# Optimization experiments

Hardware: AMD Instinct MI355X
Metric: run time of the kernel (lower is better)

## Reference

```python
import jax, jax.numpy as jnp
import numpy as np

B, H, W, C = 64, 32, 32, 256
HZ, WZ = 16, 16
N = 64          # hidden_dim = n_proposals
K = 3           # dynamic depthwise kernel size
EPS = 1e-5


def _layernorm(x, g, b):
    mu = jnp.mean(x, axis=-1, keepdims=True)
    var = jnp.var(x, axis=-1, keepdims=True)
    return (x - mu) * jax.lax.rsqrt(var + EPS) * g + b


def setup_inputs() -> dict:
    key = jax.random.key(0)
    ks = jax.random.split(key, 8)
    s = 0.02  # weight init scale
    return {
        "x_feat": jax.random.normal(ks[0], (B, H, W, C), jnp.float32),
        "z_feat": jax.random.normal(ks[1], (B, HZ, WZ, C), jnp.float32),
        "Wz": jax.random.normal(ks[2], (C, N), jnp.float32) * s,
        "bz": jnp.zeros((N,), jnp.float32),
        "Wx": jax.random.normal(ks[3], (C, N), jnp.float32) * s,
        "bx": jnp.zeros((N,), jnp.float32),
        "Wdyn": jax.random.normal(ks[4], (C, N + K), jnp.float32) * s,
        "bdyn": jnp.zeros((N + K,), jnp.float32),
        "g_norm": jnp.ones((C,), jnp.float32),
        "b_norm": jnp.zeros((C,), jnp.float32),
        "Wp": jax.random.normal(ks[5], (C, 1), jnp.float32) * s,
        "bp": jnp.zeros((1,), jnp.float32),
        "g_ln": jnp.ones((C,), jnp.float32),
        "b_ln": jnp.zeros((C,), jnp.float32),
    }


def _dysep_conv_atten(query, value, Wdyn, bdyn, g_norm, b_norm):
    # query, value: [B, N, C]
    dy = query @ Wdyn + bdyn                      # [B, N, N+K]
    w_depth = dy[:, :, :K]                        # [B, N, K] per-channel depthwise kernels
    w_point = dy[:, :, K:]                        # [B, N, N] per-sample pointwise (1x1) weights
    # depthwise conv along C with 'same' padding (torch conv1d = cross-correlation)
    vpad = jnp.pad(value, ((0, 0), (0, 0), (1, 1)))
    depth = (w_depth[..., 0:1] * vpad[:, :, 0:C]
             + w_depth[..., 1:2] * vpad[:, :, 1:C + 1]
             + w_depth[..., 2:3] * vpad[:, :, 2:C + 2])
    depth = jax.nn.relu(depth)                    # [B, N, C]
    point = jnp.einsum('bnm,bmc->bnc', w_point, depth)
    return _layernorm(point, g_norm, b_norm)


def reference(x_feat, z_feat, Wz, bz, Wx, bx, Wdyn, bdyn,
              g_norm, b_norm, Wp, bp, g_ln, b_ln):
    # kernels from template features (detached in the original: kernels.detach())
    z_core = z_feat @ Wz + bz                                   # [B,HZ,WZ,N]
    kernels = jnp.einsum('bhwn,bhwc->bnc', z_core, z_feat)      # [B,N,C]
    kernels = jax.lax.stop_gradient(kernels)

    x_n = x_feat @ Wx + bx                                      # [B,H,W,N]
    kernels_x = jnp.einsum('bhwn,bhwc->bnc', x_n, x_feat)       # [B,N,C]
    kernels_x = _dysep_conv_atten(kernels, kernels_x, Wdyn, bdyn, g_norm, b_norm)

    x_corr = jnp.einsum('bnc,bhwn->bhwc', kernels_x, x_n)       # [B,H,W,C]
    proto = kernels_x @ Wp + bp                                 # [B,N,1]
    tem = jax.nn.sigmoid(jnp.einsum('bnd,bnc->bdc', proto, kernels_x))  # [B,1,C]
    tem = tem[:, :, None, :]                                    # [B,1,1,C]
    x_corr = x_corr * tem

    return x_feat + jax.nn.relu(_layernorm(x_corr, g_ln, b_ln))
```

## Files before the change

### kernel.cpp

```cpp
#include <hip/hip_runtime.h>
#include <math.h>

#define EPSV 1e-5f

typedef __attribute__((ext_vector_type(8))) short short8;
typedef __attribute__((ext_vector_type(4))) float f32x4;

static __device__ __forceinline__ unsigned bfpack2(float lo, float hi) {
    union { float f; unsigned u; } a, b;
    a.f = lo; b.f = hi;
    unsigned ua = a.u + 0x7fffu + ((a.u >> 16) & 1u);
    unsigned ub = b.u + 0x7fffu + ((b.u >> 16) & 1u);
    return (ua >> 16) | (ub & 0xffff0000u);
}

__global__ __launch_bounds__(256) void gram(
    const float* __restrict__ Xx, const float* __restrict__ Xz,
    float* __restrict__ Gx, float* __restrict__ Gz,
    float* __restrict__ csx, float* __restrict__ csz)
{
    __shared__ __align__(16) unsigned short AT[128 * 72];
    __shared__ __align__(16) unsigned short BT[128 * 72];
    __shared__ float csr[8 * 128];
    int id = blockIdx.x;
    const float* X; float* G; float* cs; int P;
    if (id < 192) { X = Xx; G = Gx; cs = csx; P = 1024; }
    else { id -= 192; X = Xz; G = Gz; cs = csz; P = 256; }
    const int b = id & 63;
    const int tile = id >> 6;
    const int ci = (tile == 1) ? 1 : 0;
    const int cj = (tile == 0) ? 0 : 1;
    const bool diag = (tile < 2);
    const int nk = P >> 6;
    const int t = threadIdx.x;
    const int cq = (t & 31) * 4;
    const int ph = t >> 5;
    const float* Xb = X + (long)b * P * 256;

    const int w = t >> 6;
    const int wr = w >> 1, wc = w & 1;
    const int quad = (t >> 4) & 3, lane16 = t & 15;

    f32x4 acc[4][4] = {};
    float csA[4] = {0.f, 0.f, 0.f, 0.f};

    for (int kc = 0; kc < nk; ++kc) {
        const int p0 = kc * 64 + ph * 8;
        float4 va[8], vb[8];
#pragma unroll
        for (int k = 0; k < 8; ++k)
            va[k] = *(const float4*)(Xb + (long)(p0 + k) * 256 + ci * 128 + cq);
        if (!diag) {
#pragma unroll
            for (int k = 0; k < 8; ++k)
                vb[k] = *(const float4*)(Xb + (long)(p0 + k) * 256 + cj * 128 + cq);
        }
        __syncthreads();
#pragma unroll
        for (int j = 0; j < 4; ++j) {
            uint4 pk;
            pk.x = bfpack2(((const float*)&va[0])[j], ((const float*)&va[1])[j]);
            pk.y = bfpack2(((const float*)&va[2])[j], ((const float*)&va[3])[j]);
            pk.z = bfpack2(((const float*)&va[4])[j], ((const float*)&va[5])[j]);
            pk.w = bfpack2(((const float*)&va[6])[j], ((const float*)&va[7])[j]);
            *(uint4*)&AT[(cq + j) * 72 + ph * 8] = pk;
            if (diag) {
                csA[j] += ((const float*)&va[0])[j] + ((const float*)&va[1])[j]
                        + ((const float*)&va[2])[j] + ((const float*)&va[3])[j]
                        + ((const float*)&va[4])[j] + ((const float*)&va[5])[j]
                        + ((const float*)&va[6])[j] + ((const float*)&va[7])[j];
            }
        }
        if (!diag) {
#pragma unroll
            for (int j = 0; j < 4; ++j) {
                uint4 pk;
                pk.x = bfpack2(((const float*)&vb[0])[j], ((const float*)&vb[1])[j]);
                pk.y = bfpack2(((const float*)&vb[2])[j], ((const float*)&vb[3])[j]);
                pk.z = bfpack2(((const float*)&vb[4])[j], ((const float*)&vb[5])[j]);
                pk.w = bfpack2(((const float*)&vb[6])[j], ((const float*)&vb[7])[j]);
                *(uint4*)&BT[(cq + j) * 72 + ph * 8] = pk;
            }
        }
        __syncthreads();
        const unsigned short* Br = diag ? AT : BT;
#pragma unroll
        for (int ks = 0; ks < 2; ++ks) {
            const int ko = ks * 32 + quad * 8;
            short8 bfrag[4];
#pragma unroll
            for (int ni = 0; ni < 4; ++ni)
                bfrag[ni] = *(const short8*)&Br[(wc * 64 + ni * 16 + lane16) * 72 + ko];
#pragma unroll
            for (int mi = 0; mi < 4; ++mi) {
                short8 afrag = *(const short8*)&AT[(wr * 64 + mi * 16 + lane16) * 72 + ko];
#pragma unroll
                for (int ni = 0; ni < 4; ++ni)
                    acc[mi][ni] = __builtin_amdgcn_mfma_f32_16x16x32_bf16(afrag, bfrag[ni], acc[mi][ni], 0, 0, 0);
            }
        }
    }
#pragma unroll
    for (int mi = 0; mi < 4; ++mi) {
        const int rbase = ci * 128 + wr * 64 + mi * 16 + quad * 4;
#pragma unroll
        for (int ni = 0; ni < 4; ++ni) {
            const int col = cj * 128 + wc * 64 + ni * 16 + lane16;
#pragma unroll
            for (int r = 0; r < 4; ++r) {
                G[((long)(b * 256 + rbase + r)) * 256 + col] = acc[mi][ni][r];
                if (!diag)
                    G[((long)(b * 256 + col)) * 256 + rbase + r] = acc[mi][ni][r];
            }
        }
    }
    if (diag) {
#pragma unroll
        for (int j = 0; j < 4; ++j) csr[ph * 128 + cq + j] = csA[j];
        __syncthreads();
        if (t < 128) {
            float s = 0.f;
#pragma unroll
            for (int k = 0; k < 8; ++k) s += csr[k * 128 + t];
            cs[b * 256 + ci * 128 + t] = s;
        }
    }
}

__global__ __launch_bounds__(256) void proj(
    const float* __restrict__ Gx, const float* __restrict__ csx,
    const float* __restrict__ Wx, const float* __restrict__ bx,
    float* __restrict__ kxr,
    const float* __restrict__ Gz, const float* __restrict__ csz,
    const float* __restrict__ Wz, const float* __restrict__ bz,
    float* __restrict__ kern)
{
    __shared__ __align__(16) unsigned short ATW[64 * 264];
    __shared__ __align__(16) unsigned short BTC[64 * 72];
    const int t = threadIdx.x;
    const int id = blockIdx.x;
    const int b = id & 63, s = id >> 6;
    const float *G, *cs, *W, *bias; float* O;
    if (s < 4) { G = Gx; cs = csx; W = Wx; bias = bx; O = kxr; }
    else       { G = Gz; cs = csz; W = Wz; bias = bz; O = kern; }
    const int ct = s & 3;
    const int n = t & 63, ph = t >> 6;
#pragma unroll
    for (int cc = 0; cc < 4; ++cc) {
        float v[16];
#pragma unroll
        for (int k = 0; k < 16; ++k) v[k] = W[(ph * 64 + cc * 16 + k) * 64 + n];
        uint4 p0, p1;
        p0.x = bfpack2(v[0], v[1]);   p0.y = bfpack2(v[2], v[3]);
        p0.z = bfpack2(v[4], v[5]);   p0.w = bfpack2(v[6], v[7]);
        p1.x = bfpack2(v[8], v[9]);   p1.y = bfpack2(v[10], v[11]);
        p1.z = bfpack2(v[12], v[13]); p1.w = bfpack2(v[14], v[15]);
        *(uint4*)&ATW[n * 264 + ph * 64 + cc * 16]     = p0;
        *(uint4*)&ATW[n * 264 + ph * 64 + cc * 16 + 8] = p1;
    }
    const int row = t >> 2, cq = t & 3;
    const int w = t >> 6, quad = (t >> 4) & 3, lane16 = t & 15;
    const float* Grow = G + ((long)(b * 256 + ct * 64 + row)) * 256 + cq * 16;
    f32x4 acc[4] = {{0.f,0.f,0.f,0.f},{0.f,0.f,0.f,0.f},{0.f,0.f,0.f,0.f},{0.f,0.f,0.f,0.f}};
    for (int kc = 0; kc < 4; ++kc) {
        float4 g0 = *(const float4*)(Grow + kc * 64 + 0);
        float4 g1 = *(const float4*)(Grow + kc * 64 + 4);
        float4 g2 = *(const float4*)(Grow + kc * 64 + 8);
        float4 g3 = *(const float4*)(Grow + kc * 64 + 12);
        uint4 pk0, pk1;
        pk0.x = bfpack2(g0.x, g0.y); pk0.y = bfpack2(g0.z, g0.w);
        pk0.z = bfpack2(g1.x, g1.y); pk0.w = bfpack2(g1.z, g1.w);
        pk1.x = bfpack2(g2.x, g2.y); pk1.y = bfpack2(g2.z, g2.w);
        pk1.z = bfpack2(g3.x, g3.y); pk1.w = bfpack2(g3.z, g3.w);
        __syncthreads();
        *(uint4*)&BTC[row * 72 + cq * 16]     = pk0;
        *(uint4*)&BTC[row * 72 + cq * 16 + 8] = pk1;
        __syncthreads();
#pragma unroll
        for (int ks = 0; ks < 2; ++ks) {
            const int ko = ks * 32 + quad * 8;
            short8 bfrag = *(const short8*)&BTC[(w * 16 + lane16) * 72 + ko];
#pragma unroll
            for (int mi = 0; mi < 4; ++mi) {
                short8 afrag = *(const short8*)&ATW[(mi * 16 + lane16) * 264 + kc * 64 + ko];
                acc[mi] = __builtin_amdgcn_mfma_f32_16x16x32_bf16(afrag, bfrag, acc[mi], 0, 0, 0);
            }
        }
    }
    const int col = ct * 64 + w * 16 + lane16;
    const float csv = cs[b * 256 + col];
#pragma unroll
    for (int mi = 0; mi < 4; ++mi) {
        const int nrow = mi * 16 + quad * 4;
#pragma unroll
        for (int r = 0; r < 4; ++r)
            O[((long)(b * 64 + nrow + r)) * 256 + col] = acc[mi][r] + bias[nrow + r] * csv;
    }
}

__global__ __launch_bounds__(256) void dy_all(
    const float* __restrict__ kern, const float* __restrict__ Wdyn,
    const float* __restrict__ bdyn, float* __restrict__ dyb)
{
    __shared__ float Ac[16 * 64];
    __shared__ float Wc[16 * 64];
    __shared__ float Wd3[48];
    const int b = blockIdx.x, t = threadIdx.x;
    const int tr = t >> 4, tc = t & 15;
    float acc[4][4];
#pragma unroll
    for (int j = 0; j < 4; ++j) {
        float bj = bdyn[3 + tc * 4 + j];
        acc[0][j] = bj; acc[1][j] = bj; acc[2][j] = bj; acc[3][j] = bj;
    }
    const int lr = t >> 2, lc = (t & 3) * 4;
    const int wl = t >> 4, wj = (t & 15) * 4;
    const int nwd = t / 3, jwd = t - nwd * 3;
    float wdacc = 0.f;
    float4 av = *(const float4*)(kern + ((long)(b * 64 + lr)) * 256 + lc);
    float w0 = Wdyn[wl * 67 + 3 + wj + 0];
    float w1 = Wdyn[wl * 67 + 3 + wj + 1];
    float w2 = Wdyn[wl * 67 + 3 + wj + 2];
    float w3 = Wdyn[wl * 67 + 3 + wj + 3];
    float wdr = (t < 48) ? Wdyn[(t / 3) * 67 + (t % 3)] : 0.f;

    for (int c0 = 0; c0 < 256; c0 += 16) {
        Ac[(lc+0)*64 + lr] = av.x; Ac[(lc+1)*64 + lr] = av.y;
        Ac[(lc+2)*64 + lr] = av.z; Ac[(lc+3)*64 + lr] = av.w;
        Wc[wl*64 + wj+0] = w0; Wc[wl*64 + wj+1] = w1;
        Wc[wl*64 + wj+2] = w2; Wc[wl*64 + wj+3] = w3;
        if (t < 48) Wd3[t] = wdr;
        __syncthreads();
        if (c0 + 16 < 256) {
            av = *(const float4*)(kern + ((long)(b * 64 + lr)) * 256 + c0 + 16 + lc);
            w0 = Wdyn[(c0 + 16 + wl) * 67 + 3 + wj + 0];
            w1 = Wdyn[(c0 + 16 + wl) * 67 + 3 + wj + 1];
            w2 = Wdyn[(c0 + 16 + wl) * 67 + 3 + wj + 2];
            w3 = Wdyn[(c0 + 16 + wl) * 67 + 3 + wj + 3];
            if (t < 48) wdr = Wdyn[(c0 + 16 + t / 3) * 67 + (t % 3)];
        }
#pragma unroll
        for (int cl = 0; cl < 16; ++cl) {
            float4 a = *(float4*)&Ac[cl * 64 + tr * 4];
            float4 w = *(float4*)&Wc[cl * 64 + tc * 4];
            acc[0][0]+=a.x*w.x; acc[0][1]+=a.x*w.y; acc[0][2]+=a.x*w.z; acc[0][3]+=a.x*w.w;
            acc[1][0]+=a.y*w.x; acc[1][1]+=a.y*w.y; acc[1][2]+=a.y*w.z; acc[1][3]+=a.y*w.w;
            acc[2][0]+=a.z*w.x; acc[2][1]+=a.z*w.y; acc[2][2]+=a.z*w.z; acc[2][3]+=a.z*w.w;
            acc[3][0]+=a.w*w.x; acc[3][1]+=a.w*w.y; acc[3][2]+=a.w*w.z; acc[3][3]+=a.w*w.w;
        }
        if (t < 192) {
#pragma unroll
            for (int cl = 0; cl < 16; ++cl)
                wdacc += Ac[cl * 64 + nwd] * Wd3[cl * 3 + jwd];
        }
        __syncthreads();
    }
#pragma unroll
    for (int i = 0; i < 4; ++i) {
        float4 o = make_float4(acc[i][0], acc[i][1], acc[i][2], acc[i][3]);
        *(float4*)(dyb + ((long)(b * 64 + tr * 4 + i)) * 68 + tc * 4) = o;
    }
    if (t < 192) dyb[((long)(b * 64 + nwd)) * 68 + 64 + jwd] = wdacc + bdyn[jwd];
}

__global__ __launch_bounds__(256) void depthpoint(
    const float* __restrict__ dyb, const float* __restrict__ v,
    const float* __restrict__ g, const float* __restrict__ Wp,
    float* __restrict__ point, float* __restrict__ partials)
{
    __shared__ float smem[13312];
    float* wpT = smem;
    float* wd3 = smem + 4352;
    float* vt  = smem + 4608;
    float* dep = smem + 8960;
    float* rs  = vt;

    const int t = threadIdx.x;
    const int b = blockIdx.y, ct = blockIdx.x, c0 = ct * 64;
    const int tr = t >> 4, tc = t & 15;

#pragma unroll
    for (int i = 0; i < 4; ++i) {
        int idx = t + i * 256; int n = idx >> 4, m0 = (idx & 15) * 4;
        float4 w4 = *(const float4*)(dyb + ((long)(b * 64 + n)) * 68 + m0);
        wpT[(m0+0)*68 + n] = w4.x; wpT[(m0+1)*68 + n] = w4.y;
        wpT[(m0+2)*68 + n] = w4.z; wpT[(m0+3)*68 + n] = w4.w;
    }
    if (t < 64) {
        long o = ((long)(b * 64 + t)) * 68 + 64;
        wd3[t*4+0] = dyb[o+0]; wd3[t*4+1] = dyb[o+1]; wd3[t*4+2] = dyb[o+2];
    }
    {
        int m = t >> 2, lc0 = (t & 3) * 17;
#pragma unroll
        for (int k = 0; k < 17; ++k) {
            int lc = lc0 + k;
            if (lc < 66) {
                int c = c0 - 1 + lc;
                vt[m * 68 + lc] = (c >= 0 && c < 256) ? v[((long)(b * 64 + m)) * 256 + c] : 0.f;
            }
        }
    }
    __syncthreads();
#pragma unroll
    for (int im = 0; im < 4; ++im) {
        int m = tr * 4 + im;
        float w0 = wd3[m*4+0], w1 = wd3[m*4+1], w2 = wd3[m*4+2];
#pragma unroll
        for (int jc = 0; jc < 4; ++jc) {
            int cl = tc * 4 + jc;
            float d = w0 * vt[m*68 + cl] + w1 * vt[m*68 + cl + 1] + w2 * vt[m*68 + cl + 2];
            dep[m*68 + cl] = fmaxf(d, 0.f);
        }
    }
    __syncthreads();
    float acc[4][4] = {};
#pragma unroll 16
    for (int m = 0; m < 64; ++m) {
        float4 a4 = *(float4*)&wpT[m * 68 + tr * 4];
        float4 d4 = *(float4*)&dep[m * 68 + tc * 4];
        acc[0][0]+=a4.x*d4.x; acc[0][1]+=a4.x*d4.y; acc[0][2]+=a4.x*d4.z; acc[0][3]+=a4.x*d4.w;
        acc[1][0]+=a4.y*d4.x; acc[1][1]+=a4.y*d4.y; acc[1][2]+=a4.y*d4.z; acc[1][3]+=a4.y*d4.w;
        acc[2][0]+=a4.z*d4.x; acc[2][1]+=a4.z*d4.y; acc[2][2]+=a4.z*d4.z; acc[2][3]+=a4.z*d4.w;
        acc[3][0]+=a4.w*d4.x; acc[3][1]+=a4.w*d4.y; acc[3][2]+=a4.w*d4.z; acc[3][3]+=a4.w*d4.w;
    }
    int cg = c0 + tc * 4;
    float4 g4  = *(const float4*)(g + cg);
    float4 wp4 = *(const float4*)(Wp + cg);
    float gw0 = g4.x*wp4.x, gw1 = g4.y*wp4.y, gw2 = g4.z*wp4.z, gw3 = g4.w*wp4.w;
#pragma unroll
    for (int i = 0; i < 4; ++i) {
        float4 o = make_float4(acc[i][0], acc[i][1], acc[i][2], acc[i][3]);
        *(float4*)(point + ((long)(b * 64 + tr * 4 + i)) * 256 + cg) = o;
        float s  = o.x + o.y + o.z + o.w;
        float s2 = o.x*o.x + o.y*o.y + o.z*o.z + o.w*o.w;
        float dg = o.x*gw0 + o.y*gw1 + o.z*gw2 + o.w*gw3;
        rs[0*1088 + (tr*4+i)*17 + tc] = s;
        rs[1*1088 + (tr*4+i)*17 + tc] = s2;
        rs[2*1088 + (tr*4+i)*17 + tc] = dg;
    }
    __syncthreads();
    if (t < 64) {
        float s = 0.f, s2 = 0.f, dg = 0.f;
#pragma unroll
        for (int j = 0; j < 16; ++j) {
            s  += rs[t*17 + j];
            s2 += rs[1088 + t*17 + j];
            dg += rs[2176 + t*17 + j];
        }
        long base = ((long)(b * 4 + ct)) * 192;
        partials[base + t]        = s;
        partials[base + 64 + t]   = s2;
        partials[base + 128 + t]  = dg;
    }
}

__global__ __launch_bounds__(256) void lntem(
    const float* __restrict__ partials, const float* __restrict__ point,
    const float* __restrict__ g, const float* __restrict__ bta,
    const float* __restrict__ Wp, const float* __restrict__ bp,
    float* __restrict__ murr, float* __restrict__ AB)
{
    __shared__ float sA[256], sB[256];
    __shared__ float wnv[64];
    __shared__ float tot[4];
    const int b = blockIdx.x, t = threadIdx.x;
    const int c = t;
    float gc = g[c], bc = bta[c], wpc = Wp[c];
    sA[t] = gc * wpc; sB[t] = bc * wpc;
    __syncthreads();
    for (int off = 128; off >= 1; off >>= 1) {
        if (t < off) { sA[t] += sA[t+off]; sB[t] += sB[t+off]; }
        __syncthreads();
    }
    if (t == 0) { tot[0] = sA[0]; tot[1] = sB[0] + bp[0]; }
    __syncthreads();
    float Sgw = tot[0], Sbw = tot[1];

    float protoe = 0.f, mu = 0.f, rr = 0.f;
    if (t < 64) {
        float S1 = 0.f, S2 = 0.f, Sdg = 0.f;
#pragma unroll
        for (int ct = 0; ct < 4; ++ct) {
            long o = ((long)(b * 4 + ct)) * 192;
            S1 += partials[o + t]; S2 += partials[o + 64 + t]; Sdg += partials[o + 128 + t];
        }
        mu = S1 * (1.f / 256.f);
        float var = S2 * (1.f / 256.f) - mu * mu;
        rr = rsqrtf(var + EPSV);
        protoe = rr * (Sdg - mu * Sgw) + Sbw;
        wnv[t] = protoe * rr;
        murr[b * 128 + 2*t]     = rr;
        murr[b * 128 + 2*t + 1] = -mu * rr;
    }
    __syncthreads();
    sA[t] = (t < 64) ? protoe * rr * mu : 0.f;
    sB[t] = (t < 64) ? protoe : 0.f;
    __syncthreads();
    for (int off = 128; off >= 1; off >>= 1) {
        if (t < off) { sA[t] += sA[t+off]; sB[t] += sB[t+off]; }
        __syncthreads();
    }
    if (t == 0) { tot[2] = sA[0]; tot[3] = sB[0]; }
    __syncthreads();
    float Bv = tot[2], Sv = tot[3];

    const float* pcol = point + (long)b * 64 * 256 + c;
    float a0 = 0.f, a1 = 0.f, a2 = 0.f, a3 = 0.f;
#pragma unroll
    for (int n = 0; n < 64; n += 4) {
        a0 += wnv[n+0] * pcol[(n+0) * 256];
        a1 += wnv[n+1] * pcol[(n+1) * 256];
        a2 += wnv[n+2] * pcol[(n+2) * 256];
        a3 += wnv[n+3] * pcol[(n+3) * 256];
    }
    float accA = a0 + a1 + a2 + a3;
    float x = gc * (accA - Bv) + bc * Sv;
    float temv = 1.f / (1.f + expf(-x));
    AB[b * 512 + c]       = gc * temv;
    AB[b * 512 + 256 + c] = bc * temv;
}

__global__ __launch_bounds__(256) void buildM(
    const float* __restrict__ point, const float* __restrict__ murr,
    const float* __restrict__ AB, const float* __restrict__ Wx,
    const float* __restrict__ bx,
    unsigned short* __restrict__ MT, float* __restrict__ svec)
{
    __shared__ float ks_s[64 * 68];
    __shared__ float wt_s[64 * 68];
    const int t = threadIdx.x;
    const int id = blockIdx.x;
    const int b = id & 63, mt = id >> 6;
    {
        const int n = t >> 2, q = t & 3;
        const float rn = murr[b * 128 + 2 * n], qn = murr[b * 128 + 2 * n + 1];
        const float* prow = point + ((long)(b * 64 + n)) * 256 + mt * 64 + q * 16;
        const float* Arow = AB + b * 512 + mt * 64 + q * 16;
#pragma unroll
        for (int j = 0; j < 4; ++j) {
            float4 p4 = *(const float4*)(prow + j * 4);
            float4 A4 = *(const float4*)(Arow + j * 4);
            float4 B4 = *(const float4*)(Arow + 256 + j * 4);
            float4 kv;
            kv.x = (p4.x * rn + qn) * A4.x + B4.x;
            kv.y = (p4.y * rn + qn) * A4.y + B4.y;
            kv.z = (p4.z * rn + qn) * A4.z + B4.z;
            kv.w = (p4.w * rn + qn) * A4.w + B4.w;
            *(float4*)&ks_s[n * 68 + q * 16 + j * 4] = kv;
        }
    }
    __syncthreads();
    if (t < 64) {
        float sv = 0.f;
#pragma unroll
        for (int n2 = 0; n2 < 64; ++n2) sv += bx[n2] * ks_s[n2 * 68 + t];
        svec[b * 256 + mt * 64 + t] = sv;
    }
    const int tr = t >> 4, tc = t & 15;
    const int nw = t & 63, ph = t >> 6;
    for (int cc = 0; cc < 4; ++cc) {
        float wv[16];
#pragma unroll
        for (int k = 0; k < 16; ++k) wv[k] = Wx[(cc * 64 + ph * 16 + k) * 64 + nw];
        __syncthreads();
#pragma unroll
        for (int k = 0; k < 16; ++k) wt_s[nw * 68 + ph * 16 + k] = wv[k];
        __syncthreads();
        float a2[4][4] = {};
#pragma unroll 16
        for (int n2 = 0; n2 < 64; ++n2) {
            float4 a4 = *(float4*)&ks_s[n2 * 68 + tr * 4];
            float4 w4 = *(float4*)&wt_s[n2 * 68 + tc * 4];
            a2[0][0]+=a4.x*w4.x; a2[0][1]+=a4.x*w4.y; a2[0][2]+=a4.x*w4.z; a2[0][3]+=a4.x*w4.w;
            a2[1][0]+=a4.y*w4.x; a2[1][1]+=a4.y*w4.y; a2[1][2]+=a4.y*w4.z; a2[1][3]+=a4.y*w4.w;
            a2[2][0]+=a4.z*w4.x; a2[2][1]+=a4.z*w4.y; a2[2][2]+=a4.z*w4.z; a2[2][3]+=a4.z*w4.w;
            a2[3][0]+=a4.w*w4.x; a2[3][1]+=a4.w*w4.y; a2[3][2]+=a4.w*w4.z; a2[3][3]+=a4.w*w4.w;
        }
#pragma unroll
        for (int i = 0; i < 4; ++i) {
            uint2 pk;
            pk.x = bfpack2(a2[i][0], a2[i][1]);
            pk.y = bfpack2(a2[i][2], a2[i][3]);
            *(uint2*)&MT[((long)(b * 256 + mt * 64 + tr * 4 + i)) * 256 + cc * 64 + tc * 4] = pk;
        }
    }
}

__global__ __launch_bounds__(256) void final2(
    const float* __restrict__ xf, const unsigned short* __restrict__ MT,
    const float* __restrict__ svec, const float* __restrict__ g,
    const float* __restrict__ bt, float* __restrict__ out)
{
    __shared__ __align__(16) float SlArr[32 * 132];
    __shared__ float red1[128], red2[128];
    __shared__ float muS[32], rrS[32];
    unsigned short* XT = (unsigned short*)SlArr;
    float* Sl = SlArr;
    const int t = threadIdx.x;
    const int id = blockIdx.x;
    const int b = id & 63, pt = id >> 6;
    const int w = t >> 6, quad = (t >> 4) & 3, lane16 = t & 15;
    const float* Xb = xf + ((long)(b * 1024 + pt * 32)) * 256;
    {
        const int p = t >> 3, q = t & 7;
#pragma unroll
        for (int i = 0; i < 8; ++i) {
            const int c = q * 32 + i * 4;
            float4 v = *(const float4*)(Xb + (long)p * 256 + c);
            uint2 pk;
            pk.x = bfpack2(v.x, v.y);
            pk.y = bfpack2(v.z, v.w);
            *(uint2*)&XT[p * 264 + c] = pk;
        }
    }
    __syncthreads();
    f32x4 acc[2][4] = {};
    const unsigned short* Mb = MT + (long)b * 65536;
    for (int ks = 0; ks < 8; ++ks) {
        const int ko = ks * 32 + quad * 8;
        short8 bf4[4], af2[2];
#pragma unroll
        for (int ni = 0; ni < 4; ++ni)
            bf4[ni] = *(const short8*)(Mb + (long)(w * 64 + ni * 16 + lane16) * 256 + ko);
#pragma unroll
        for (int mi = 0; mi < 2; ++mi)
            af2[mi] = *(const short8*)&XT[(mi * 16 + lane16) * 264 + ko];
#pragma unroll
        for (int mi = 0; mi < 2; ++mi)
#pragma unroll
            for (int ni = 0; ni < 4; ++ni)
                acc[mi][ni] = __builtin_amdgcn_mfma_f32_16x16x32_bf16(af2[mi], bf4[ni], acc[mi][ni], 0, 0, 0);
    }
    float sv4[4];
#pragma unroll
    for (int ni = 0; ni < 4; ++ni) sv4[ni] = svec[b * 256 + w * 64 + ni * 16 + lane16];
#pragma unroll
    for (int mi = 0; mi < 2; ++mi)
#pragma unroll
        for (int r = 0; r < 4; ++r) {
            float s1 = 0.f, s2 = 0.f;
#pragma unroll
            for (int ni = 0; ni < 4; ++ni) {
                float v2 = acc[mi][ni][r] + sv4[ni];
                acc[mi][ni][r] = v2;
                s1 += v2; s2 += v2 * v2;
            }
#pragma unroll
            for (int m = 1; m <= 8; m <<= 1) {
                s1 += __shfl_xor(s1, m);
                s2 += __shfl_xor(s2, m);
            }
            if (lane16 == 0) {
                red1[(mi * 16 + quad * 4 + r) * 4 + w] = s1;
                red2[(mi * 16 + quad * 4 + r) * 4 + w] = s2;
            }
        }
    __syncthreads();
    if (t < 32) {
        float sa = red1[t*4] + red1[t*4+1] + red1[t*4+2] + red1[t*4+3];
        float sb = red2[t*4] + red2[t*4+1] + red2[t*4+2] + red2[t*4+3];
        float m = sa * (1.f / 256.f);
        muS[t] = m;
        rrS[t] = rsqrtf(sb * (1.f / 256.f) - m * m + EPSV);
    }
#pragma unroll
    for (int h = 0; h < 2; ++h) {
        __syncthreads();
        if ((w >> 1) == h) {
            const int chalf = (w & 1) * 64;
#pragma unroll
            for (int mi = 0; mi < 2; ++mi)
#pragma unroll
                for (int ni = 0; ni < 4; ++ni)
#pragma unroll
                    for (int r = 0; r < 4; ++r)
                        Sl[(mi * 16 + quad * 4 + r) * 132 + chalf + ni * 16 + lane16] = acc[mi][ni][r];
        }
        __syncthreads();
        {
            const int p = t >> 3, q = t & 7;
            const float m = muS[p], rr = rrS[p];
            const long grow = ((long)(b * 1024 + pt * 32 + p)) * 256;
#pragma unroll
            for (int j = 0; j < 4; ++j) {
                const int cl = q * 16 + j * 4;
                const int c = h * 128 + cl;
                float4 a  = *(float4*)&Sl[p * 132 + cl];
                float4 g4 = *(const float4*)(g + c);
                float4 b4 = *(const float4*)(bt + c);
                float4 xv = *(const float4*)(xf + grow + c);
                float4 o;
                o.x = xv.x + fmaxf((a.x - m) * rr * g4.x + b4.x, 0.f);
                o.y = xv.y + fmaxf((a.y - m) * rr * g4.y + b4.y, 0.f);
                o.z = xv.z + fmaxf((a.z - m) * rr * g4.z + b4.z, 0.f);
                o.w = xv.w + fmaxf((a.w - m) * rr * g4.w + b4.w, 0.f);
                *(float4*)(out + grow + c) = o;
            }
        }
    }
}

extern "C" void kernel_launch(void* const* d_in, const int* in_sizes, int n_in,
                              void* d_out, int out_size, void* d_ws, size_t ws_size,
                              hipStream_t stream)
{
    (void)in_sizes; (void)n_in; (void)out_size; (void)ws_size;
    const float* x_feat = (const float*)d_in[0];
    const float* z_feat = (const float*)d_in[1];
    const float* Wz     = (const float*)d_in[2];
    const float* bz     = (const float*)d_in[3];
    const float* Wx     = (const float*)d_in[4];
    const float* bx     = (const float*)d_in[5];
    const float* Wdyn   = (const float*)d_in[6];
    const float* bdyn   = (const float*)d_in[7];
    const float* g_norm = (const float*)d_in[8];
    const float* b_norm = (const float*)d_in[9];
    const float* Wp     = (const float*)d_in[10];
    const float* bp     = (const float*)d_in[11];
    const float* g_ln   = (const float*)d_in[12];
    const float* b_ln   = (const float*)d_in[13];
    float* out = (float*)d_out;

    float* ws       = (float*)d_ws;
    float* Gx       = ws;
    float* Gz       = Gx + 4194304;
    float* kern     = Gz + 4194304;
    float* kxr      = kern + 1048576;
    float* point    = kxr + 1048576;
    float* dyb      = point + 1048576;
    float* partials = dyb + 278528;
    float* murr     = partials + 49152;
    float* AB       = murr + 8192;
    float* csx      = AB + 32768;
    float* csz      = csx + 16384;
    float* svec     = csz + 16384;
    unsigned short* MT = (unsigned short*)(svec + 16384);

    gram<<<384, 256, 0, stream>>>(x_feat, z_feat, Gx, Gz, csx, csz);
    proj<<<512, 256, 0, stream>>>(Gx, csx, Wx, bx, kxr, Gz, csz, Wz, bz, kern);
    dy_all<<<64, 256, 0, stream>>>(kern, Wdyn, bdyn, dyb);
    depthpoint<<<dim3(4, 64), 256, 0, stream>>>(dyb, kxr, g_norm, Wp, point, partials);
    lntem<<<64, 256, 0, stream>>>(partials, point, g_norm, b_norm, Wp, bp, murr, AB);
    buildM<<<256, 256, 0, stream>>>(point, murr, AB, Wx, bx, MT, svec);
    final2<<<2048, 256, 0, stream>>>(x_feat, MT, svec, g_ln, b_ln, out);
}
```

Before: 297.8 us.

## Fuse mid-pipeline kernels into one per-batch megakernel and prefetch gram loads

Five middle kernels (proj, dy_all, depthpoint, lntem, buildM) are merged into one 64-block kernel that keeps the intermediates in a large shared-memory pool, so workspace round trips and launch gaps disappear. The gram kernel now prefetches the next K-chunk into registers while the MFMAs run. final2 keeps the x tile in registers for the residual add instead of reloading it, and writes the full 256-column slice in one pass. The cost is that the mid stage drops from hundreds of blocks to 64, leaving most CUs idle during that phase, and its roughly 146 KB shared allocation limits occupancy to one block per CU.

Result: slower. 337.7 us (+13.4%).

```diff
diff --git a/kernel.cpp b/kernel.cpp
--- a/kernel.cpp
+++ b/kernel.cpp
@@ -44,9 +44,9 @@
     f32x4 acc[4][4] = {};
     float csA[4] = {0.f, 0.f, 0.f, 0.f};
 
-    for (int kc = 0; kc < nk; ++kc) {
-        const int p0 = kc * 64 + ph * 8;
-        float4 va[8], vb[8];
+    float4 va[8], vb[8];
+    {
+        const int p0 = ph * 8;
 #pragma unroll
         for (int k = 0; k < 8; ++k)
             va[k] = *(const float4*)(Xb + (long)(p0 + k) * 256 + ci * 128 + cq);
@@ -55,6 +55,9 @@
             for (int k = 0; k < 8; ++k)
                 vb[k] = *(const float4*)(Xb + (long)(p0 + k) * 256 + cj * 128 + cq);
         }
+    }
+
+    for (int kc = 0; kc < nk; ++kc) {
         __syncthreads();
 #pragma unroll
         for (int j = 0; j < 4; ++j) {
@@ -83,6 +86,17 @@
             }
         }
         __syncthreads();
+        if (kc + 1 < nk) {
+            const int p0 = (kc + 1) * 64 + ph * 8;
+#pragma unroll
+            for (int k = 0; k < 8; ++k)
+                va[k] = *(const float4*)(Xb + (long)(p0 + k) * 256 + ci * 128 + cq);
+            if (!diag) {
+#pragma unroll
+                for (int k = 0; k < 8; ++k)
+                    vb[k] = *(const float4*)(Xb + (long)(p0 + k) * 256 + cj * 128 + cq);
+            }
+        }
         const unsigned short* Br = diag ? AT : BT;
 #pragma unroll
         for (int ks = 0; ks < 2; ++ks) {
@@ -127,362 +141,327 @@
     }
 }
 
-__global__ __launch_bounds__(256) void proj(
+__global__ __launch_bounds__(256) void megamid(
     const float* __restrict__ Gx, const float* __restrict__ csx,
     const float* __restrict__ Wx, const float* __restrict__ bx,
-    float* __restrict__ kxr,
     const float* __restrict__ Gz, const float* __restrict__ csz,
     const float* __restrict__ Wz, const float* __restrict__ bz,
-    float* __restrict__ kern)
+    const float* __restrict__ Wdyn, const float* __restrict__ bdyn,
+    const float* __restrict__ g_norm, const float* __restrict__ b_norm,
+    const float* __restrict__ Wp, const float* __restrict__ bp,
+    float* __restrict__ point, unsigned short* __restrict__ MT,
+    float* __restrict__ svec)
 {
-    __shared__ __align__(16) unsigned short ATW[64 * 264];
-    __shared__ __align__(16) unsigned short BTC[64 * 72];
+    __shared__ __align__(16) unsigned char pool[149760];
+    float* KXR          = (float*)pool;
+    unsigned short* ATW = (unsigned short*)(pool + 66816);
+    unsigned short* BTC = (unsigned short*)(pool + 100608);
+    float* SLICE        = (float*)(pool + 109824);
+    float* WC2          = (float*)(pool + 128256);
+    float* WD3L         = (float*)(pool + 145664);
+    float* DYB          = (float*)(pool + 66816);
+    float* WPT          = (float*)(pool + 84224);
+    float* DEP          = (float*)(pool + 101632);
+    float* WD3S         = (float*)(pool + 119040);
+    float* RS           = (float*)(pool + 120064);
+    float* SRA          = (float*)(pool + 101632);
+    float* SRB          = (float*)(pool + 102656);
+    float* WNV          = (float*)(pool + 103680);
+    float* TOT          = (float*)(pool + 103936);
+    float* KS           = (float*)(pool + 66816);
+    float* WT           = (float*)(pool + 84224);
+    float* PSUM         = (float*)(pool + 146432);
+    float* MURR         = (float*)(pool + 147200);
+    float* ABL          = (float*)(pool + 147712);
+
+    const int b = blockIdx.x;
     const int t = threadIdx.x;
-    const int id = blockIdx.x;
-    const int b = id & 63, s = id >> 6;
-    const float *G, *cs, *W, *bias; float* O;
-    if (s < 4) { G = Gx; cs = csx; W = Wx; bias = bx; O = kxr; }
-    else       { G = Gz; cs = csz; W = Wz; bias = bz; O = kern; }
-    const int ct = s & 3;
-    const int n = t & 63, ph = t >> 6;
-#pragma unroll
-    for (int cc = 0; cc < 4; ++cc) {
-        float v[16];
-#pragma unroll
-        for (int k = 0; k < 16; ++k) v[k] = W[(ph * 64 + cc * 16 + k) * 64 + n];
-        uint4 p0, p1;
-        p0.x = bfpack2(v[0], v[1]);   p0.y = bfpack2(v[2], v[3]);
-        p0.z = bfpack2(v[4], v[5]);   p0.w = bfpack2(v[6], v[7]);
-        p1.x = bfpack2(v[8], v[9]);   p1.y = bfpack2(v[10], v[11]);
-        p1.z = bfpack2(v[12], v[13]); p1.w = bfpack2(v[14], v[15]);
-        *(uint4*)&ATW[n * 264 + ph * 64 + cc * 16]     = p0;
-        *(uint4*)&ATW[n * 264 + ph * 64 + cc * 16 + 8] = p1;
-    }
-    const int row = t >> 2, cq = t & 3;
     const int w = t >> 6, quad = (t >> 4) & 3, lane16 = t & 15;
-    const float* Grow = G + ((long)(b * 256 + ct * 64 + row)) * 256 + cq * 16;
-    f32x4 acc[4] = {{0.f,0.f,0.f,0.f},{0.f,0.f,0.f,0.f},{0.f,0.f,0.f,0.f},{0.f,0.f,0.f,0.f}};
-    for (int kc = 0; kc < 4; ++kc) {
-        float4 g0 = *(const float4*)(Grow + kc * 64 + 0);
-        float4 g1 = *(const float4*)(Grow + kc * 64 + 4);
-        float4 g2 = *(const float4*)(Grow + kc * 64 + 8);
-        float4 g3 = *(const float4*)(Grow + kc * 64 + 12);
-        uint4 pk0, pk1;
-        pk0.x = bfpack2(g0.x, g0.y); pk0.y = bfpack2(g0.z, g0.w);
-        pk0.z = bfpack2(g1.x, g1.y); pk0.w = bfpack2(g1.z, g1.w);
-        pk1.x = bfpack2(g2.x, g2.y); pk1.y = bfpack2(g2.z, g2.w);
-        pk1.z = bfpack2(g3.x, g3.y); pk1.w = bfpack2(g3.z, g3.w);
-        __syncthreads();
-        *(uint4*)&BTC[row * 72 + cq * 16]     = pk0;
-        *(uint4*)&BTC[row * 72 + cq * 16 + 8] = pk1;
-        __syncthreads();
-#pragma unroll
-        for (int ks = 0; ks < 2; ++ks) {
-            const int ko = ks * 32 + quad * 8;
-            short8 bfrag = *(const short8*)&BTC[(w * 16 + lane16) * 72 + ko];
-#pragma unroll
-            for (int mi = 0; mi < 4; ++mi) {
-                short8 afrag = *(const short8*)&ATW[(mi * 16 + lane16) * 264 + kc * 64 + ko];
-                acc[mi] = __builtin_amdgcn_mfma_f32_16x16x32_bf16(afrag, bfrag, acc[mi], 0, 0, 0);
-            }
-        }
-    }
-    const int col = ct * 64 + w * 16 + lane16;
-    const float csv = cs[b * 256 + col];
-#pragma unroll
-    for (int mi = 0; mi < 4; ++mi) {
-        const int nrow = mi * 16 + quad * 4;
-#pragma unroll
-        for (int r = 0; r < 4; ++r)
-            O[((long)(b * 64 + nrow + r)) * 256 + col] = acc[mi][r] + bias[nrow + r] * csv;
-    }
-}
-
-__global__ __launch_bounds__(256) void dy_all(
-    const float* __restrict__ kern, const float* __restrict__ Wdyn,
-    const float* __restrict__ bdyn, float* __restrict__ dyb)
-{
-    __shared__ float Ac[16 * 64];
-    __shared__ float Wc[16 * 64];
-    __shared__ float Wd3[48];
-    const int b = blockIdx.x, t = threadIdx.x;
     const int tr = t >> 4, tc = t & 15;
-    float acc[4][4];
+    const int nwd3 = t / 3, jwd3 = t - nwd3 * 3;
+
+    if (t < 192) PSUM[t] = 0.f;
+
+    float adv[4][4];
 #pragma unroll
     for (int j = 0; j < 4; ++j) {
         float bj = bdyn[3 + tc * 4 + j];
-        acc[0][j] = bj; acc[1][j] = bj; acc[2][j] = bj; acc[3][j] = bj;
-    }
-    const int lr = t >> 2, lc = (t & 3) * 4;
-    const int wl = t >> 4, wj = (t & 15) * 4;
-    const int nwd = t / 3, jwd = t - nwd * 3;
+        adv[0][j] = bj; adv[1][j] = bj; adv[2][j] = bj; adv[3][j] = bj;
+    }
     float wdacc = 0.f;
-    float4 av = *(const float4*)(kern + ((long)(b * 64 + lr)) * 256 + lc);
-    float w0 = Wdyn[wl * 67 + 3 + wj + 0];
-    float w1 = Wdyn[wl * 67 + 3 + wj + 1];
-    float w2 = Wdyn[wl * 67 + 3 + wj + 2];
-    float w3 = Wdyn[wl * 67 + 3 + wj + 3];
-    float wdr = (t < 48) ? Wdyn[(t / 3) * 67 + (t % 3)] : 0.f;
-
-    for (int c0 = 0; c0 < 256; c0 += 16) {
-        Ac[(lc+0)*64 + lr] = av.x; Ac[(lc+1)*64 + lr] = av.y;
-        Ac[(lc+2)*64 + lr] = av.z; Ac[(lc+3)*64 + lr] = av.w;
-        Wc[wl*64 + wj+0] = w0; Wc[wl*64 + wj+1] = w1;
-        Wc[wl*64 + wj+2] = w2; Wc[wl*64 + wj+3] = w3;
-        if (t < 48) Wd3[t] = wdr;
-        __syncthreads();
-        if (c0 + 16 < 256) {
-            av = *(const float4*)(kern + ((long)(b * 64 + lr)) * 256 + c0 + 16 + lc);
-            w0 = Wdyn[(c0 + 16 + wl) * 67 + 3 + wj + 0];
-            w1 = Wdyn[(c0 + 16 + wl) * 67 + 3 + wj + 1];
-            w2 = Wdyn[(c0 + 16 + wl) * 67 + 3 + wj + 2];
-            w3 = Wdyn[(c0 + 16 + wl) * 67 + 3 + wj + 3];
-            if (t < 48) wdr = Wdyn[(c0 + 16 + t / 3) * 67 + (t % 3)];
-        }
-#pragma unroll
-        for (int cl = 0; cl < 16; ++cl) {
-            float4 a = *(float4*)&Ac[cl * 64 + tr * 4];
-            float4 w = *(float4*)&Wc[cl * 64 + tc * 4];
-            acc[0][0]+=a.x*w.x; acc[0][1]+=a.x*w.y; acc[0][2]+=a.x*w.z; acc[0][3]+=a.x*w.w;
-            acc[1][0]+=a.y*w.x; acc[1][1]+=a.y*w.y; acc[1][2]+=a.y*w.z; acc[1][3]+=a.y*w.w;
-            acc[2][0]+=a.z*w.x; acc[2][1]+=a.z*w.y; acc[2][2]+=a.z*w.z; acc[2][3]+=a.z*w.w;
-            acc[3][0]+=a.w*w.x; acc[3][1]+=a.w*w.y; acc[3][2]+=a.w*w.z; acc[3][3]+=a.w*w.w;
-        }
-        if (t < 192) {
-#pragma unroll
-            for (int cl = 0; cl < 16; ++cl)
-                wdacc += Ac[cl * 64 + nwd] * Wd3[cl * 3 + jwd];
-        }
-        __syncthreads();
-    }
+
+    for (int path = 0; path < 2; ++path) {
+        const float* G    = path ? Gz : Gx;
+        const float* cs   = path ? csz : csx;
+        const float* W    = path ? Wz : Wx;
+        const float* bias = path ? bz : bx;
+        __syncthreads();
+        {
+            const int n = t & 63, ph2 = t >> 6;
+#pragma unroll
+            for (int cc = 0; cc < 4; ++cc) {
+                float v[16];
+#pragma unroll
+                for (int k = 0; k < 16; ++k) v[k] = W[(ph2 * 64 + cc * 16 + k) * 64 + n];
+                uint4 p0, p1;
+                p0.x = bfpack2(v[0], v[1]);   p0.y = bfpack2(v[2], v[3]);
+                p0.z = bfpack2(v[4], v[5]);   p0.w = bfpack2(v[6], v[7]);
+                p1.x = bfpack2(v[8], v[9]);   p1.y = bfpack2(v[10], v[11]);
+                p1.z = bfpack2(v[12], v[13]); p1.w = bfpack2(v[14], v[15]);
+                *(uint4*)&ATW[n * 264 + ph2 * 64 + cc * 16]     = p0;
+                *(uint4*)&ATW[n * 264 + ph2 * 64 + cc * 16 + 8] = p1;
+            }
+        }
+        __syncthreads();
+        for (int ct = 0; ct < 4; ++ct) {
+            f32x4 pacc[4] = {{0.f,0.f,0.f,0.f},{0.f,0.f,0.f,0.f},{0.f,0.f,0.f,0.f},{0.f,0.f,0.f,0.f}};
+            const int row = t >> 2, cqq = t & 3;
+            const float* Grow = G + ((long)(b * 256 + ct * 64 + row)) * 256 + cqq * 16;
+            for (int kc = 0; kc < 4; ++kc) {
+                float4 g0 = *(const float4*)(Grow + kc * 64 + 0);
+                float4 g1 = *(const float4*)(Grow + kc * 64 + 4);
+                float4 g2 = *(const float4*)(Grow + kc * 64 + 8);
+                float4 g3 = *(const float4*)(Grow + kc * 64 + 12);
+                uint4 pk0, pk1;
+                pk0.x = bfpack2(g0.x, g0.y); pk0.y = bfpack2(g0.z, g0.w);
+                pk0.z = bfpack2(g1.x, g1.y); pk0.w = bfpack2(g1.z, g1.w);
+                pk1.x = bfpack2(g2.x, g2.y); pk1.y = bfpack2(g2.z, g2.w);
+                pk1.z = bfpack2(g3.x, g3.y); pk1.w = bfpack2(g3.z, g3.w);
+                __syncthreads();
+                *(uint4*)&BTC[row * 72 + cqq * 16]     = pk0;
+                *(uint4*)&BTC[row * 72 + cqq * 16 + 8] = pk1;
+                __syncthreads();
+#pragma unroll
+                for (int ks = 0; ks < 2; ++ks) {
+                    const int ko = ks * 32 + quad * 8;
+                    short8 bfrag = *(const short8*)&BTC[(w * 16 + lane16) * 72 + ko];
+#pragma unroll
+                    for (int mi = 0; mi < 4; ++mi) {
+                        short8 afrag = *(const short8*)&ATW[(mi * 16 + lane16) * 264 + kc * 64 + ko];
+                        pacc[mi] = __builtin_amdgcn_mfma_f32_16x16x32_bf16(afrag, bfrag, pacc[mi], 0, 0, 0);
+                    }
+                }
+            }
+            const int col = ct * 64 + w * 16 + lane16;
+            const float csv = cs[b * 256 + col];
+            if (path == 0) {
+#pragma unroll
+                for (int mi = 0; mi < 4; ++mi) {
+                    const int nrow = mi * 16 + quad * 4;
+#pragma unroll
+                    for (int r = 0; r < 4; ++r)
+                        KXR[(nrow + r) * 261 + col] = pacc[mi][r] + bias[nrow + r] * csv;
+                }
+            } else {
+                const int cloc = w * 16 + lane16;
+#pragma unroll
+                for (int mi = 0; mi < 4; ++mi) {
+                    const int nrow = mi * 16 + quad * 4;
+#pragma unroll
+                    for (int r = 0; r < 4; ++r)
+                        SLICE[cloc * 72 + nrow + r] = pacc[mi][r] + bias[nrow + r] * csv;
+                }
+                {
+                    const int m = t & 63, clg = t >> 6;
+#pragma unroll
+                    for (int j = 0; j < 16; ++j) {
+                        int cl = clg * 16 + j;
+                        WC2[cl * 68 + m] = Wdyn[((long)(ct * 64 + cl)) * 67 + 3 + m];
+                    }
+                    if (t < 192) WD3L[t] = Wdyn[((long)(ct * 64 + nwd3)) * 67 + jwd3];
+                }
+                __syncthreads();
+#pragma unroll 16
+                for (int cl = 0; cl < 64; ++cl) {
+                    float4 a  = *(float4*)&SLICE[cl * 72 + tr * 4];
+                    float4 wv = *(float4*)&WC2[cl * 68 + tc * 4];
+                    adv[0][0]+=a.x*wv.x; adv[0][1]+=a.x*wv.y; adv[0][2]+=a.x*wv.z; adv[0][3]+=a.x*wv.w;
+                    adv[1][0]+=a.y*wv.x; adv[1][1]+=a.y*wv.y; adv[1][2]+=a.y*wv.z; adv[1][3]+=a.y*wv.w;
+                    adv[2][0]+=a.z*wv.x; adv[2][1]+=a.z*wv.y; adv[2][2]+=a.z*wv.z; adv[2][3]+=a.z*wv.w;
+                    adv[3][0]+=a.w*wv.x; adv[3][1]+=a.w*wv.y; adv[3][2]+=a.w*wv.z; adv[3][3]+=a.w*wv.w;
+                }
+                if (t < 192) {
+#pragma unroll 16
+                    for (int cl = 0; cl < 64; ++cl)
+                        wdacc += SLICE[cl * 72 + nwd3] * WD3L[cl * 3 + jwd3];
+                }
+            }
+        }
+    }
+    __syncthreads();
 #pragma unroll
     for (int i = 0; i < 4; ++i) {
-        float4 o = make_float4(acc[i][0], acc[i][1], acc[i][2], acc[i][3]);
-        *(float4*)(dyb + ((long)(b * 64 + tr * 4 + i)) * 68 + tc * 4) = o;
-    }
-    if (t < 192) dyb[((long)(b * 64 + nwd)) * 68 + 64 + jwd] = wdacc + bdyn[jwd];
-}
-
-__global__ __launch_bounds__(256) void depthpoint(
-    const float* __restrict__ dyb, const float* __restrict__ v,
-    const float* __restrict__ g, const float* __restrict__ Wp,
-    float* __restrict__ point, float* __restrict__ partials)
-{
-    __shared__ float smem[13312];
-    float* wpT = smem;
-    float* wd3 = smem + 4352;
-    float* vt  = smem + 4608;
-    float* dep = smem + 8960;
-    float* rs  = vt;
-
-    const int t = threadIdx.x;
-    const int b = blockIdx.y, ct = blockIdx.x, c0 = ct * 64;
-    const int tr = t >> 4, tc = t & 15;
-
+        float4 o = make_float4(adv[i][0], adv[i][1], adv[i][2], adv[i][3]);
+        *(float4*)&DYB[(tr * 4 + i) * 68 + tc * 4] = o;
+    }
+    if (t < 192) DYB[nwd3 * 68 + 64 + jwd3] = wdacc + bdyn[jwd3];
+    __syncthreads();
 #pragma unroll
     for (int i = 0; i < 4; ++i) {
         int idx = t + i * 256; int n = idx >> 4, m0 = (idx & 15) * 4;
-        float4 w4 = *(const float4*)(dyb + ((long)(b * 64 + n)) * 68 + m0);
-        wpT[(m0+0)*68 + n] = w4.x; wpT[(m0+1)*68 + n] = w4.y;
-        wpT[(m0+2)*68 + n] = w4.z; wpT[(m0+3)*68 + n] = w4.w;
+        float4 w4 = *(float4*)&DYB[n * 68 + m0];
+        WPT[(m0+0)*68 + n] = w4.x; WPT[(m0+1)*68 + n] = w4.y;
+        WPT[(m0+2)*68 + n] = w4.z; WPT[(m0+3)*68 + n] = w4.w;
     }
     if (t < 64) {
-        long o = ((long)(b * 64 + t)) * 68 + 64;
-        wd3[t*4+0] = dyb[o+0]; wd3[t*4+1] = dyb[o+1]; wd3[t*4+2] = dyb[o+2];
+        WD3S[t*4+0] = DYB[t*68 + 64]; WD3S[t*4+1] = DYB[t*68 + 65]; WD3S[t*4+2] = DYB[t*68 + 66];
+    }
+    __syncthreads();
+    for (int ct = 0; ct < 4; ++ct) {
+        const int c0 = ct * 64;
+#pragma unroll
+        for (int im = 0; im < 4; ++im) {
+            int m = tr * 4 + im;
+            float w0 = WD3S[m*4+0], w1 = WD3S[m*4+1], w2 = WD3S[m*4+2];
+#pragma unroll
+            for (int jc = 0; jc < 4; ++jc) {
+                int cl = tc * 4 + jc, c = c0 + cl;
+                float vm1 = (c > 0)   ? KXR[m * 261 + c - 1] : 0.f;
+                float v0  =            KXR[m * 261 + c];
+                float vp1 = (c < 255) ? KXR[m * 261 + c + 1] : 0.f;
+                DEP[m * 68 + cl] = fmaxf(w0 * vm1 + w1 * v0 + w2 * vp1, 0.f);
+            }
+        }
+        __syncthreads();
+        float pa[4][4] = {};
+#pragma unroll 16
+        for (int m = 0; m < 64; ++m) {
+            float4 a4 = *(float4*)&WPT[m * 68 + tr * 4];
+            float4 d4 = *(float4*)&DEP[m * 68 + tc * 4];
+            pa[0][0]+=a4.x*d4.x; pa[0][1]+=a4.x*d4.y; pa[0][2]+=a4.x*d4.z; pa[0][3]+=a4.x*d4.w;
+            pa[1][0]+=a4.y*d4.x; pa[1][1]+=a4.y*d4.y; pa[1][2]+=a4.y*d4.z; pa[1][3]+=a4.y*d4.w;
+            pa[2][0]+=a4.z*d4.x; pa[2][1]+=a4.z*d4.y; pa[2][2]+=a4.z*d4.z; pa[2][3]+=a4.z*d4.w;
+            pa[3][0]+=a4.w*d4.x; pa[3][1]+=a4.w*d4.y; pa[3][2]+=a4.w*d4.z; pa[3][3]+=a4.w*d4.w;
+        }
+        int cg = c0 + tc * 4;
+        float4 g4  = *(const float4*)(g_norm + cg);
+        float4 wp4 = *(const float4*)(Wp + cg);
+        float gw0 = g4.x*wp4.x, gw1 = g4.y*wp4.y, gw2 = g4.z*wp4.z, gw3 = g4.w*wp4.w;
+#pragma unroll
+        for (int i = 0; i < 4; ++i) {
+            float4 o = make_float4(pa[i][0], pa[i][1], pa[i][2], pa[i][3]);
+            *(float4*)(point + ((long)(b * 64 + tr * 4 + i)) * 256 + cg) = o;
+            float s  = o.x + o.y + o.z + o.w;
+            float s2 = o.x*o.x + o.y*o.y + o.z*o.z + o.w*o.w;
+            float dg = o.x*gw0 + o.y*gw1 + o.z*gw2 + o.w*gw3;
+            RS[0*1088 + (tr*4+i)*17 + tc] = s;
+            RS[1*1088 + (tr*4+i)*17 + tc] = s2;
+            RS[2*1088 + (tr*4+i)*17 + tc] = dg;
+        }
+        __syncthreads();
+        if (t < 64) {
+            float s = 0.f, s2 = 0.f, dg = 0.f;
+#pragma unroll
+            for (int j = 0; j < 16; ++j) {
+                s  += RS[t*17 + j];
+                s2 += RS[1088 + t*17 + j];
+                dg += RS[2176 + t*17 + j];
+            }
+            PSUM[t] += s; PSUM[64 + t] += s2; PSUM[128 + t] += dg;
+        }
+        __syncthreads();
     }
     {
-        int m = t >> 2, lc0 = (t & 3) * 17;
-#pragma unroll
-        for (int k = 0; k < 17; ++k) {
-            int lc = lc0 + k;
-            if (lc < 66) {
-                int c = c0 - 1 + lc;
-                vt[m * 68 + lc] = (c >= 0 && c < 256) ? v[((long)(b * 64 + m)) * 256 + c] : 0.f;
-            }
-        }
-    }
-    __syncthreads();
-#pragma unroll
-    for (int im = 0; im < 4; ++im) {
-        int m = tr * 4 + im;
-        float w0 = wd3[m*4+0], w1 = wd3[m*4+1], w2 = wd3[m*4+2];
-#pragma unroll
-        for (int jc = 0; jc < 4; ++jc) {
-            int cl = tc * 4 + jc;
-            float d = w0 * vt[m*68 + cl] + w1 * vt[m*68 + cl + 1] + w2 * vt[m*68 + cl + 2];
-            dep[m*68 + cl] = fmaxf(d, 0.f);
-        }
-    }
-    __syncthreads();
-    float acc[4][4] = {};
+        const int c = t;
+        float gc = g_norm[c], bc = b_norm[c], wpc = Wp[c];
+        SRA[t] = gc * wpc; SRB[t] = bc * wpc;
+        __syncthreads();
+        for (int off = 128; off >= 1; off >>= 1) {
+            if (t < off) { SRA[t] += SRA[t+off]; SRB[t] += SRB[t+off]; }
+            __syncthreads();
+        }
+        if (t == 0) { TOT[0] = SRA[0]; TOT[1] = SRB[0] + bp[0]; }
+        __syncthreads();
+        float Sgw = TOT[0], Sbw = TOT[1];
+
+        float protoe = 0.f, mu = 0.f, rr = 0.f;
+        if (t < 64) {
+            float S1 = PSUM[t], S2 = PSUM[64 + t], Sdg = PSUM[128 + t];
+            mu = S1 * (1.f / 256.f);
+            float var = S2 * (1.f / 256.f) - mu * mu;
+            rr = rsqrtf(var + EPSV);
+            protoe = rr * (Sdg - mu * Sgw) + Sbw;
+            WNV[t] = protoe * rr;
+            MURR[2*t] = rr; MURR[2*t + 1] = -mu * rr;
+        }
+        __syncthreads();
+        SRA[t] = (t < 64) ? protoe * rr * mu : 0.f;
+        SRB[t] = (t < 64) ? protoe : 0.f;
+        __syncthreads();
+        for (int off = 128; off >= 1; off >>= 1) {
+            if (t < off) { SRA[t] += SRA[t+off]; SRB[t] += SRB[t+off]; }
+            __syncthreads();
+        }
+        if (t == 0) { TOT[2] = SRA[0]; TOT[3] = SRB[0]; }
+        __syncthreads();
+        float Bv = TOT[2], Sv = TOT[3];
+
+        const float* pcol = point + (long)b * 64 * 256 + c;
+        float a0 = 0.f, a1 = 0.f, a2 = 0.f, a3 = 0.f;
+#pragma unroll
+        for (int n = 0; n < 64; n += 4) {
+            a0 += WNV[n+0] * pcol[(n+0) * 256];
+            a1 += WNV[n+1] * pcol[(n+1) * 256];
+            a2 += WNV[n+2] * pcol[(n+2) * 256];
+            a3 += WNV[n+3] * pcol[(n+3) * 256];
+        }
+        float accA = a0 + a1 + a2 + a3;
+        float x = gc * (accA - Bv) + bc * Sv;
+        float temv = 1.f / (1.f + expf(-x));
+        ABL[c] = gc * temv; ABL[256 + c] = bc * temv;
+    }
+    for (int mt = 0; mt < 4; ++mt) {
+        __syncthreads();
+        {
+            const int n = t >> 2, q = t & 3;
+            const float rn = MURR[2 * n], qn = MURR[2 * n + 1];
+            const float* prow = point + ((long)(b * 64 + n)) * 256 + mt * 64 + q * 16;
+#pragma unroll
+            for (int j = 0; j < 4; ++j) {
+                float4 p4 = *(const float4*)(prow + j * 4);
+                float4 A4 = *(float4*)&ABL[mt * 64 + q * 16 + j * 4];
+                float4 B4 = *(float4*)&ABL[256 + mt * 64 + q * 16 + j * 4];
+                float4 kv;
+                kv.x = (p4.x * rn + qn) * A4.x + B4.x;
+                kv.y = (p4.y * rn + qn) * A4.y + B4.y;
+                kv.z = (p4.z * rn + qn) * A4.z + B4.z;
+                kv.w = (p4.w * rn + qn) * A4.w + B4.w;
+                *(float4*)&KS[n * 68 + q * 16 + j * 4] = kv;
+            }
+        }
+        __syncthreads();
+        if (t < 64) {
+            float sv = 0.f;
+#pragma unroll
+            for (int n2 = 0; n2 < 64; ++n2) sv += bx[n2] * KS[n2 * 68 + t];
+            svec[b * 256 + mt * 64 + t] = sv;
+        }
+        const int nw = t & 63, ph2 = t >> 6;
+        for (int cc = 0; cc < 4; ++cc) {
+            float wv[16];
+#pragma unroll
+            for (int k = 0; k < 16; ++k) wv[k] = Wx[(cc * 64 + ph2 * 16 + k) * 64 + nw];
+            __syncthreads();
+#pragma unroll
+            for (int k = 0; k < 16; ++k) WT[nw * 68 + ph2 * 16 + k] = wv[k];
+            __syncthreads();
+            float a2[4][4] = {};
 #pragma unroll 16
-    for (int m = 0; m < 64; ++m) {
-        float4 a4 = *(float4*)&wpT[m * 68 + tr * 4];
-        float4 d4 = *(float4*)&dep[m * 68 + tc * 4];
-        acc[0][0]+=a4.x*d4.x; acc[0][1]+=a4.x*d4.y; acc[0][2]+=a4.x*d4.z; acc[0][3]+=a4.x*d4.w;
-        acc[1][0]+=a4.y*d4.x; acc[1][1]+=a4.y*d4.y; acc[1][2]+=a4.y*d4.z; acc[1][3]+=a4.y*d4.w;
-        acc[2][0]+=a4.z*d4.x; acc[2][1]+=a4.z*d4.y; acc[2][2]+=a4.z*d4.z; acc[2][3]+=a4.z*d4.w;
-        acc[3][0]+=a4.w*d4.x; acc[3][1]+=a4.w*d4.y; acc[3][2]+=a4.w*d4.z; acc[3][3]+=a4.w*d4.w;
-    }
-    int cg = c0 + tc * 4;
-    float4 g4  = *(const float4*)(g + cg);
-    float4 wp4 = *(const float4*)(Wp + cg);
-    float gw0 = g4.x*wp4.x, gw1 = g4.y*wp4.y, gw2 = g4.z*wp4.z, gw3 = g4.w*wp4.w;
-#pragma unroll
-    for (int i = 0; i < 4; ++i) {
-        float4 o = make_float4(acc[i][0], acc[i][1], acc[i][2], acc[i][3]);
-        *(float4*)(point + ((long)(b * 64 + tr * 4 + i)) * 256 + cg) = o;
-        float s  = o.x + o.y + o.z + o.w;
-        float s2 = o.x*o.x + o.y*o.y + o.z*o.z + o.w*o.w;
-        float dg = o.x*gw0 + o.y*gw1 + o.z*gw2 + o.w*gw3;
-        rs[0*1088 + (tr*4+i)*17 + tc] = s;
-        rs[1*1088 + (tr*4+i)*17 + tc] = s2;
-        rs[2*1088 + (tr*4+i)*17 + tc] = dg;
-    }
-    __syncthreads();
-    if (t < 64) {
-        float s = 0.f, s2 = 0.f, dg = 0.f;
-#pragma unroll
-        for (int j = 0; j < 16; ++j) {
-            s  += rs[t*17 + j];
-            s2 += rs[1088 + t*17 + j];
-            dg += rs[2176 + t*17 + j];
-        }
-        long base = ((long)(b * 4 + ct)) * 192;
-        partials[base + t]        = s;
-        partials[base + 64 + t]   = s2;
-        partials[base + 128 + t]  = dg;
-    }
-}
-
-__global__ __launch_bounds__(256) void lntem(
-    const float* __restrict__ partials, const float* __restrict__ point,
-    const float* __restrict__ g, const float* __restrict__ bta,
-    const float* __restrict__ Wp, const float* __restrict__ bp,
-    float* __restrict__ murr, float* __restrict__ AB)
-{
-    __shared__ float sA[256], sB[256];
-    __shared__ float wnv[64];
-    __shared__ float tot[4];
-    const int b = blockIdx.x, t = threadIdx.x;
-    const int c = t;
-    float gc = g[c], bc = bta[c], wpc = Wp[c];
-    sA[t] = gc * wpc; sB[t] = bc * wpc;
-    __syncthreads();
-    for (int off = 128; off >= 1; off >>= 1) {
-        if (t < off) { sA[t] += sA[t+off]; sB[t] += sB[t+off]; }
-        __syncthreads();
-    }
-    if (t == 0) { tot[0] = sA[0]; tot[1] = sB[0] + bp[0]; }
-    __syncthreads();
-    float Sgw = tot[0], Sbw = tot[1];
-
-    float protoe = 0.f, mu = 0.f, rr = 0.f;
-    if (t < 64) {
-        float S1 = 0.f, S2 = 0.f, Sdg = 0.f;
-#pragma unroll
-        for (int ct = 0; ct < 4; ++ct) {
-            long o = ((long)(b * 4 + ct)) * 192;
-            S1 += partials[o + t]; S2 += partials[o + 64 + t]; Sdg += partials[o + 128 + t];
-        }
-        mu = S1 * (1.f / 256.f);
-        float var = S2 * (1.f / 256.f) - mu * mu;
-        rr = rsqrtf(var + EPSV);
-        protoe = rr * (Sdg - mu * Sgw) + Sbw;
-        wnv[t] = protoe * rr;
-        murr[b * 128 + 2*t]     = rr;
-        murr[b * 128 + 2*t + 1] = -mu * rr;
-    }
-    __syncthreads();
-    sA[t] = (t < 64) ? protoe * rr * mu : 0.f;
-    sB[t] = (t < 64) ? protoe : 0.f;
-    __syncthreads();
-    for (int off = 128; off >= 1; off >>= 1) {
-        if (t < off) { sA[t] += sA[t+off]; sB[t] += sB[t+off]; }
-        __syncthreads();
-    }
-    if (t == 0) { tot[2] = sA[0]; tot[3] = sB[0]; }
-    __syncthreads();
-    float Bv = tot[2], Sv = tot[3];
-
-    const float* pcol = point + (long)b * 64 * 256 + c;
-    float a0 = 0.f, a1 = 0.f, a2 = 0.f, a3 = 0.f;
-#pragma unroll
-    for (int n = 0; n < 64; n += 4) {
-        a0 += wnv[n+0] * pcol[(n+0) * 256];
-        a1 += wnv[n+1] * pcol[(n+1) * 256];
-        a2 += wnv[n+2] * pcol[(n+2) * 256];
-        a3 += wnv[n+3] * pcol[(n+3) * 256];
-    }
-    float accA = a0 + a1 + a2 + a3;
-    float x = gc * (accA - Bv) + bc * Sv;
-    float temv = 1.f / (1.f + expf(-x));
-    AB[b * 512 + c]       = gc * temv;
-    AB[b * 512 + 256 + c] = bc * temv;
-}
-
-__global__ __launch_bounds__(256) void buildM(
-    const float* __restrict__ point, const float* __restrict__ murr,
-    const float* __restrict__ AB, const float* __restrict__ Wx,
-    const float* __restrict__ bx,
-    unsigned short* __restrict__ MT, float* __restrict__ svec)
-{
-    __shared__ float ks_s[64 * 68];
-    __shared__ float wt_s[64 * 68];
-    const int t = threadIdx.x;
-    const int id = blockIdx.x;
-    const int b = id & 63, mt = id >> 6;
-    {
-        const int n = t >> 2, q = t & 3;
-        const float rn = murr[b * 128 + 2 * n], qn = murr[b * 128 + 2 * n + 1];
-        const float* prow = point + ((long)(b * 64 + n)) * 256 + mt * 64 + q * 16;
-        const float* Arow = AB + b * 512 + mt * 64 + q * 16;
-#pragma unroll
-        for (int j = 0; j < 4; ++j) {
-            float4 p4 = *(const float4*)(prow + j * 4);
-            float4 A4 = *(const float4*)(Arow + j * 4);
-            float4 B4 = *(const float4*)(Arow + 256 + j * 4);
-            float4 kv;
-            kv.x = (p4.x * rn + qn) * A4.x + B4.x;
-            kv.y = (p4.y * rn + qn) * A4.y + B4.y;
-            kv.z = (p4.z * rn + qn) * A4.z + B4.z;
-            kv.w = (p4.w * rn + qn) * A4.w + B4.w;
-            *(float4*)&ks_s[n * 68 + q * 16 + j * 4] = kv;
-        }
-    }
-    __syncthreads();
-    if (t < 64) {
-        float sv = 0.f;
-#pragma unroll
-        for (int n2 = 0; n2 < 64; ++n2) sv += bx[n2] * ks_s[n2 * 68 + t];
-        svec[b * 256 + mt * 64 + t] = sv;
-    }
-    const int tr = t >> 4, tc = t & 15;
-    const int nw = t & 63, ph = t >> 6;
-    for (int cc = 0; cc < 4; ++cc) {
-        float wv[16];
-#pragma unroll
-        for (int k = 0; k < 16; ++k) wv[k] = Wx[(cc * 64 + ph * 16 + k) * 64 + nw];
-        __syncthreads();
-#pragma unroll
-        for (int k = 0; k < 16; ++k) wt_s[nw * 68 + ph * 16 + k] = wv[k];
-        __syncthreads();
-        float a2[4][4] = {};
-#pragma unroll 16
-        for (int n2 = 0; n2 < 64; ++n2) {
-            float4 a4 = *(float4*)&ks_s[n2 * 68 + tr * 4];
-            float4 w4 = *(float4*)&wt_s[n2 * 68 + tc * 4];
-            a2[0][0]+=a4.x*w4.x; a2[0][1]+=a4.x*w4.y; a2[0][2]+=a4.x*w4.z; a2[0][3]+=a4.x*w4.w;
-            a2[1][0]+=a4.y*w4.x; a2[1][1]+=a4.y*w4.y; a2[1][2]+=a4.y*w4.z; a2[1][3]+=a4.y*w4.w;
-            a2[2][0]+=a4.z*w4.x; a2[2][1]+=a4.z*w4.y; a2[2][2]+=a4.z*w4.z; a2[2][3]+=a4.z*w4.w;
-            a2[3][0]+=a4.w*w4.x; a2[3][1]+=a4.w*w4.y; a2[3][2]+=a4.w*w4.z; a2[3][3]+=a4.w*w4.w;
-        }
-#pragma unroll
-        for (int i = 0; i < 4; ++i) {
-            uint2 pk;
-            pk.x = bfpack2(a2[i][0], a2[i][1]);
-            pk.y = bfpack2(a2[i][2], a2[i][3]);
-            *(uint2*)&MT[((long)(b * 256 + mt * 64 + tr * 4 + i)) * 256 + cc * 64 + tc * 4] = pk;
+            for (int n2 = 0; n2 < 64; ++n2) {
+                float4 a4 = *(float4*)&KS[n2 * 68 + tr * 4];
+                float4 w4 = *(float4*)&WT[n2 * 68 + tc * 4];
+                a2[0][0]+=a4.x*w4.x; a2[0][1]+=a4.x*w4.y; a2[0][2]+=a4.x*w4.z; a2[0][3]+=a4.x*w4.w;
+                a2[1][0]+=a4.y*w4.x; a2[1][1]+=a4.y*w4.y; a2[1][2]+=a4.y*w4.z; a2[1][3]+=a4.y*w4.w;
+                a2[2][0]+=a4.z*w4.x; a2[2][1]+=a4.z*w4.y; a2[2][2]+=a4.z*w4.z; a2[2][3]+=a4.z*w4.w;
+                a2[3][0]+=a4.w*w4.x; a2[3][1]+=a4.w*w4.y; a2[3][2]+=a4.w*w4.z; a2[3][3]+=a4.w*w4.w;
+            }
+#pragma unroll
+            for (int i = 0; i < 4; ++i) {
+                uint2 pk;
+                pk.x = bfpack2(a2[i][0], a2[i][1]);
+                pk.y = bfpack2(a2[i][2], a2[i][3]);
+                *(uint2*)&MT[((long)(b * 256 + mt * 64 + tr * 4 + i)) * 256 + cc * 64 + tc * 4] = pk;
+            }
         }
     }
 }
@@ -492,27 +471,29 @@
     const float* __restrict__ svec, const float* __restrict__ g,
     const float* __restrict__ bt, float* __restrict__ out)
 {
-    __shared__ __align__(16) float SlArr[32 * 132];
+    __shared__ __align__(16) float Sl[32 * 260];
     __shared__ float red1[128], red2[128];
     __shared__ float muS[32], rrS[32];
-    unsigned short* XT = (unsigned short*)SlArr;
-    float* Sl = SlArr;
+    unsigned short* XT = (unsigned short*)Sl;
     const int t = threadIdx.x;
     const int id = blockIdx.x;
     const int b = id & 63, pt = id >> 6;
     const int w = t >> 6, quad = (t >> 4) & 3, lane16 = t & 15;
+    const int p = t >> 3, q = t & 7;
     const float* Xb = xf + ((long)(b * 1024 + pt * 32)) * 256;
-    {
-        const int p = t >> 3, q = t & 7;
-#pragma unroll
-        for (int i = 0; i < 8; ++i) {
-            const int c = q * 32 + i * 4;
-            float4 v = *(const float4*)(Xb + (long)p * 256 + c);
-            uint2 pk;
-            pk.x = bfpack2(v.x, v.y);
-            pk.y = bfpack2(v.z, v.w);
-            *(uint2*)&XT[p * 264 + c] = pk;
-        }
+    float4 xv[8];
+#pragma unroll
+    for (int i = 0; i < 8; ++i) {
+        const int c = q * 4 + i * 32;
+        xv[i] = *(const float4*)(Xb + (long)p * 256 + c);
+    }
+#pragma unroll
+    for (int i = 0; i < 8; ++i) {
+        const int c = q * 4 + i * 32;
+        uint2 pk;
+        pk.x = bfpack2(xv[i].x, xv[i].y);
+        pk.y = bfpack2(xv[i].z, xv[i].w);
+        *(uint2*)&XT[p * 264 + c] = pk;
     }
     __syncthreads();
     f32x4 acc[2][4] = {};
@@ -564,39 +545,30 @@
         muS[t] = m;
         rrS[t] = rsqrtf(sb * (1.f / 256.f) - m * m + EPSV);
     }
-#pragma unroll
-    for (int h = 0; h < 2; ++h) {
-        __syncthreads();
-        if ((w >> 1) == h) {
-            const int chalf = (w & 1) * 64;
-#pragma unroll
-            for (int mi = 0; mi < 2; ++mi)
-#pragma unroll
-                for (int ni = 0; ni < 4; ++ni)
-#pragma unroll
-                    for (int r = 0; r < 4; ++r)
-                        Sl[(mi * 16 + quad * 4 + r) * 132 + chalf + ni * 16 + lane16] = acc[mi][ni][r];
-        }
-        __syncthreads();
-        {
-            const int p = t >> 3, q = t & 7;
-            const float m = muS[p], rr = rrS[p];
-            const long grow = ((long)(b * 1024 + pt * 32 + p)) * 256;
-#pragma unroll
-            for (int j = 0; j < 4; ++j) {
-                const int cl = q * 16 + j * 4;
-                const int c = h * 128 + cl;
-                float4 a  = *(float4*)&Sl[p * 132 + cl];
-                float4 g4 = *(const float4*)(g + c);
-                float4 b4 = *(const float4*)(bt + c);
-                float4 xv = *(const float4*)(xf + grow + c);
-                float4 o;
-                o.x = xv.x + fmaxf((a.x - m) * rr * g4.x + b4.x, 0.f);
-                o.y = xv.y + fmaxf((a.y - m) * rr * g4.y + b4.y, 0.f);
-                o.z = xv.z + fmaxf((a.z - m) * rr * g4.z + b4.z, 0.f);
-                o.w = xv.w + fmaxf((a.w - m) * rr * g4.w + b4.w, 0.f);
-                *(float4*)(out + grow + c) = o;
-            }
+    __syncthreads();
+#pragma unroll
+    for (int mi = 0; mi < 2; ++mi)
+#pragma unroll
+        for (int ni = 0; ni < 4; ++ni)
+#pragma unroll
+            for (int r = 0; r < 4; ++r)
+                Sl[(mi * 16 + quad * 4 + r) * 260 + w * 64 + ni * 16 + lane16] = acc[mi][ni][r];
+    __syncthreads();
+    {
+        const float m = muS[p], rr = rrS[p];
+        const long grow = ((long)(b * 1024 + pt * 32 + p)) * 256;
+#pragma unroll
+        for (int i = 0; i < 8; ++i) {
+            const int c = q * 4 + i * 32;
+            float4 a  = *(float4*)&Sl[p * 260 + c];
+            float4 g4 = *(const float4*)(g + c);
+            float4 b4 = *(const float4*)(bt + c);
+            float4 o;
+            o.x = xv[i].x + fmaxf((a.x - m) * rr * g4.x + b4.x, 0.f);
+            o.y = xv[i].y + fmaxf((a.y - m) * rr * g4.y + b4.y, 0.f);
+            o.z = xv[i].z + fmaxf((a.z - m) * rr * g4.z + b4.z, 0.f);
+            o.w = xv[i].w + fmaxf((a.w - m) * rr * g4.w + b4.w, 0.f);
+            *(float4*)(out + grow + c) = o;
         }
     }
 }
@@ -625,23 +597,15 @@
     float* ws       = (float*)d_ws;
     float* Gx       = ws;
     float* Gz       = Gx + 4194304;
-    float* kern     = Gz + 4194304;
-    float* kxr      = kern + 1048576;
-    float* point    = kxr + 1048576;
-    float* dyb      = point + 1048576;
-    float* partials = dyb + 278528;
-    float* murr     = partials + 49152;
-    float* AB       = murr + 8192;
-    float* csx      = AB + 32768;
+    float* point    = Gz + 4194304;
+    float* csx      = point + 1048576;
     float* csz      = csx + 16384;
     float* svec     = csz + 16384;
     unsigned short* MT = (unsigned short*)(svec + 16384);
 
     gram<<<384, 256, 0, stream>>>(x_feat, z_feat, Gx, Gz, csx, csz);
-    proj<<<512, 256, 0, stream>>>(Gx, csx, Wx, bx, kxr, Gz, csz, Wz, bz, kern);
-    dy_all<<<64, 256, 0, stream>>>(kern, Wdyn, bdyn, dyb);
-    depthpoint<<<dim3(4, 64), 256, 0, stream>>>(dyb, kxr, g_norm, Wp, point, partials);
-    lntem<<<64, 256, 0, stream>>>(partials, point, g_norm, b_norm, Wp, bp, murr, AB);
-    buildM<<<256, 256, 0, stream>>>(point, murr, AB, Wx, bx, MT, svec);
+    megamid<<<64, 256, 0, stream>>>(Gx, csx, Wx, bx, Gz, csz, Wz, bz,
+                                    Wdyn, bdyn, g_norm, b_norm, Wp, bp,
+                                    point, MT, svec);
     final2<<<2048, 256, 0, stream>>>(x_feat, MT, svec, g_ln, b_ln, out);
 }
```
